# Kernel tuning notes

Measured on AMD Instinct MI355X. Metric: run time of the kernel, lower is better.

Reference implementation:

```python
import jax, jax.numpy as jnp
import numpy as np


def _ramp_filter(sino):
    # Ram-Lak ramp filter along detector columns (last axis), applied in Fourier
    # space. Equivalent to projector.filter_projections, vectorized over batch.
    n = sino.shape[-1]
    ramp = (2.0 * jnp.abs(jnp.fft.fftfreq(n))).astype(sino.dtype)  # [C]
    f = jnp.fft.fft(sino, axis=-1)
    return jnp.real(jnp.fft.ifft(f * ramp, axis=-1)).astype(sino.dtype)


def _fbp(sino):
    # sino: [B, V, R, C] -> image [B, R, C, C]
    B, V, R, C = sino.shape
    filt = _ramp_filter(sino)
    npix = C
    half = (npix - 1) / 2.0
    coords = jnp.arange(npix, dtype=sino.dtype) - half
    X = coords[None, :]          # image x, broadcasts to [npix, npix]
    Y = coords[:, None]          # image y
    angles = jnp.linspace(0.0, np.pi, V, endpoint=False).astype(sino.dtype)
    dcenter = (C - 1) / 2.0

    def body(acc, inputs):
        proj, theta = inputs                      # proj: [B, R, C]
        t = X * jnp.cos(theta) + Y * jnp.sin(theta) + dcenter  # [npix, npix]
        t = jnp.clip(t, 0.0, C - 1)
        i0 = jnp.floor(t).astype(jnp.int32)
        i1 = jnp.minimum(i0 + 1, C - 1)
        w = (t - i0).astype(proj.dtype)
        g0 = proj[:, :, i0]                       # gather -> [B, R, npix, npix]
        g1 = proj[:, :, i1]
        return acc + g0 * (1.0 - w) + g1 * w, None

    init = jnp.zeros((B, R, npix, npix), sino.dtype)
    projT = jnp.moveaxis(filt, 1, 0)              # [V, B, R, C]
    acc, _ = jax.lax.scan(body, init, (projT, angles))
    img = acc * (np.pi / V)
    return jnp.maximum(img, 0.0)                  # img[img < 0] = 0


def setup_inputs() -> dict:
    key = jax.random.key(0)
    B, V, R, C = 2, 180, 32, 512
    sino = jax.random.normal(key, (B, V, R, C), dtype=jnp.float32)
    return {"sino": sino}


def reference(sino):
    return _fbp(sino)
```

## Files before the change

### kernel.cpp

```cpp
#include <hip/hip_runtime.h>
#include <math.h>

#ifndef M_PI
#define M_PI 3.14159265358979323846
#endif

#define BB 2
#define VV 180
#define RR 32
#define CC 512
#define NPIX 512

#define PADL 106
#define PW 724
#define TCEN 362

#define SH3 8
#define CHP 2
#define NCHP 45

#define SH 16
#define CH2 6
#define NCHUNK2 30

#define TAB_OFF 2048
#define FILT_OFF 2048

__global__ void precompute_kernel(float* __restrict__ ws) {
    int j = blockIdx.x * blockDim.x + threadIdx.x;
    if (j < 512) {
        float s = 0.f;
        for (int m = 1; m < 512; ++m) {
            int p = (m * j) & 511;
            float ang = (float)(2.0 * M_PI / 512.0) * (float)p;
            int mm = m < 512 - m ? m : 512 - m;
            float ramp = 2.0f * (float)mm * (1.0f / 512.0f);
            s += ramp * cosf(ang);
        }
        s *= (1.0f / 512.0f);
        s *= (float)(M_PI / (double)VV);
        ws[j] = s;
        ws[j + 512] = s;
    }
    if (j < VV) {
        float th = (float)((double)j * M_PI / 180.0);
        float c = cosf(th), sn = sinf(th);
        ws[1024 + j] = c;
        ws[1024 + 180 + j] = sn;
        ws[1408 + 2 * j] = c;
        ws[1408 + 2 * j + 1] = sn;
    }
}

__global__ __launch_bounds__(128) void conv_table_kernel(const float* __restrict__ sino,
                                                         const float* __restrict__ ws,
                                                         float* __restrict__ table) {
    __shared__ float rows_s[16 * 512];
    __shared__ float h_s[1024];
    int t = threadIdx.x;
    int blk = blockIdx.x;
    int bv = blk >> 1;
    int half = blk & 1;
    int b = bv / 180;
    int v = bv - b * 180;

    const float4* src4 = (const float4*)(sino + (((size_t)bv * 32) + (size_t)half * 16) * 512);
    float4* rows4 = (float4*)rows_s;
    for (int i = t; i < 2048; i += 128) rows4[i] = src4[i];
    for (int i = t; i < 1024; i += 128) h_s[i] = ws[i];
    __syncthreads();

    int wave = t >> 6;
    int lane = t & 63;
    int row0 = wave * 8;

    float acc[8][8];
#pragma unroll
    for (int j = 0; j < 8; ++j)
#pragma unroll
        for (int i = 0; i < 8; ++i) acc[j][i] = 0.f;

    for (int k = 0; k < 512; k += 4) {
        float4 rv[8];
#pragma unroll
        for (int j = 0; j < 8; ++j)
            rv[j] = *(const float4*)&rows_s[(row0 + j) * 512 + k];
#pragma unroll
        for (int u = 0; u < 4; ++u) {
            float hv[8];
            int base = lane - (k + u) + 512;
#pragma unroll
            for (int i = 0; i < 8; ++i) hv[i] = h_s[base + 64 * i];
#pragma unroll
            for (int j = 0; j < 8; ++j) {
                float rj = (u == 0) ? rv[j].x : (u == 1) ? rv[j].y : (u == 2) ? rv[j].z : rv[j].w;
#pragma unroll
                for (int i = 0; i < 8; ++i) acc[j][i] = fmaf(rj, hv[i], acc[j][i]);
            }
        }
    }

    __syncthreads();
#pragma unroll
    for (int j = 0; j < 8; ++j)
#pragma unroll
        for (int i = 0; i < 8; ++i)
            rows_s[(row0 + j) * 512 + lane + 64 * i] = acc[j][i];
    __syncthreads();

    int p = (v < 90) ? v : v - 90;
    size_t halfByte = (v < 90) ? 0 : 8;
    for (int jj = 0; jj < 16; ++jj) {
        const float* fr = rows_s + jj * 512;
        int slice = b * 32 + half * 16 + jj;
        char* trow = (char*)table + (((size_t)slice * 90 + p) * PW) * 16 + halfByte;
        for (int cx = t; cx < PW; cx += 128) {
            int s0 = cx - PADL;
            int i0 = min(max(s0, 0), 511);
            int i1 = min(max(s0 + 1, 0), 511);
            float f0 = fr[i0];
            float d = fr[i1] - f0;
            float m = (float)(cx - TCEN);
            *(float2*)(trow + (size_t)cx * 16) = make_float2(fmaf(-m, d, f0), d);
        }
    }
}

__global__ __launch_bounds__(256, 6) void backproj_pair_kernel(const float4* __restrict__ tab,
                                                               const float2* __restrict__ trigp,
                                                               float* __restrict__ out) {
    __shared__ float4 pbuf[CHP * PW];
    __shared__ float2 trig_s[90];
    int t = threadIdx.x;
    int slice = blockIdx.y;
    int strip = blockIdx.x;
    int y0 = strip * SH3;
    const float4* tslice = tab + (size_t)slice * (90 * PW);

    for (int i = t; i < 90; i += 256) trig_s[i] = trigp[i];

    float xc = (float)t + 0.5f;

    float acc0[SH3], acc1[SH3], acc2[SH3], acc3[SH3];
#pragma unroll
    for (int j = 0; j < SH3; ++j) { acc0[j] = 0.f; acc1[j] = 0.f; acc2[j] = 0.f; acc3[j] = 0.f; }

    for (int chunk = 0; chunk < NCHP; ++chunk) {
        __syncthreads();
        const float4* src = tslice + chunk * (CHP * PW);
        for (int i = t; i < CHP * PW; i += 256) pbuf[i] = src[i];
        __syncthreads();
#pragma unroll
        for (int pa = 0; pa < CHP; ++pa) {
            float2 cs = trig_s[chunk * CHP + pa];
            const float4* pb = pbuf + pa * PW + TCEN;
#pragma unroll
            for (int j = 0; j < SH3; ++j) {
                float ycj = (float)(y0 + j) + 0.5f;
                float ysm  = fmaf(ycj, cs.y, -0.5f);
                float yccm = fmaf(-ycj, cs.x, -0.5f);
                float ua  = fmaf(xc, cs.x, ysm);
                float ub  = fmaf(xc, cs.y, yccm);
                float uma = -1.0f - ua;
                float umb = -1.0f - ub;
                int ma  = (int)floorf(ua);
                int mma = (int)floorf(uma);
                int mb  = (int)floorf(ub);
                int mmb = (int)floorf(umb);
                float4 qa  = pb[ma];
                float4 qma = pb[mma];
                float4 qb  = pb[mb];
                float4 qmb = pb[mmb];
                acc0[j] = fmaf(ua,  qa.y,  acc0[j]) + qa.x;
                acc1[j] = fmaf(ua,  qa.w,  acc1[j]) + qa.z;
                acc2[j] = fmaf(uma, qma.y, acc2[j]) + qma.x;
                acc3[j] = fmaf(uma, qma.w, acc3[j]) + qma.z;
                acc1[j] = fmaf(ub,  qb.y,  acc1[j]) + qb.x;
                acc2[j] = fmaf(ub,  qb.w,  acc2[j]) + qb.z;
                acc3[j] = fmaf(umb, qmb.y, acc3[j]) + qmb.x;
                acc0[j] = fmaf(umb, qmb.w, acc0[j]) + qmb.z;
            }
        }
    }

    int px = 256 + t;
    size_t sbase = (size_t)slice * (512 * 512);
#pragma unroll
    for (int j = 0; j < SH3; ++j) {
        int py = 256 + y0 + j;
        float v0 = acc0[j], v1 = acc1[j], v2 = acc2[j], v3 = acc3[j];
        out[sbase + (size_t)py * 512 + px]                   = v0 > 0.f ? v0 : 0.f;
        out[sbase + (size_t)px * 512 + (511 - py)]           = v1 > 0.f ? v1 : 0.f;
        out[sbase + (size_t)(511 - py) * 512 + (511 - px)]   = v2 > 0.f ? v2 : 0.f;
        out[sbase + (size_t)(511 - px) * 512 + py]           = v3 > 0.f ? v3 : 0.f;
    }
}

__global__ __launch_bounds__(128) void conv_kernel(const float* __restrict__ sino,
                                                   const float* __restrict__ ws,
                                                   float* __restrict__ filt) {
    __shared__ float rows_s[16 * 512];
    __shared__ float h_s[1024];
    int t = threadIdx.x;
    int blk = blockIdx.x;
    int bv = blk >> 1;
    int half = blk & 1;
    int b = bv / 180;
    int v = bv - b * 180;

    const float4* src4 = (const float4*)(sino + (((size_t)bv * 32) + (size_t)half * 16) * 512);
    float4* rows4 = (float4*)rows_s;
    for (int i = t; i < 2048; i += 128) rows4[i] = src4[i];
    for (int i = t; i < 1024; i += 128) h_s[i] = ws[i];
    __syncthreads();

    int wave = t >> 6;
    int lane = t & 63;
    int row0 = wave * 8;

    float acc[8][8];
#pragma unroll
    for (int j = 0; j < 8; ++j)
#pragma unroll
        for (int i = 0; i < 8; ++i) acc[j][i] = 0.f;

    for (int k = 0; k < 512; k += 4) {
        float4 rv[8];
#pragma unroll
        for (int j = 0; j < 8; ++j)
            rv[j] = *(const float4*)&rows_s[(row0 + j) * 512 + k];
#pragma unroll
        for (int u = 0; u < 4; ++u) {
            float hv[8];
            int base = lane - (k + u) + 512;
#pragma unroll
            for (int i = 0; i < 8; ++i) hv[i] = h_s[base + 64 * i];
#pragma unroll
            for (int j = 0; j < 8; ++j) {
                float rj = (u == 0) ? rv[j].x : (u == 1) ? rv[j].y : (u == 2) ? rv[j].z : rv[j].w;
#pragma unroll
                for (int i = 0; i < 8; ++i) acc[j][i] = fmaf(rj, hv[i], acc[j][i]);
            }
        }
    }

#pragma unroll
    for (int j = 0; j < 8; ++j) {
        int r = half * 16 + row0 + j;
        float* dst = filt + (((size_t)b * 32 + r) * 180 + v) * 512;
#pragma unroll
        for (int i = 0; i < 8; ++i) dst[lane + 64 * i] = acc[j][i];
    }
}

__global__ __launch_bounds__(256) void backproj_kernel(const float* __restrict__ filt,
                                                       const float* __restrict__ trig,
                                                       float* __restrict__ out) {
    __shared__ float2 pbuf[CH2][PW];
    __shared__ float trig_s[360];
    int t = threadIdx.x;
    int slice = blockIdx.y;
    int strip = blockIdx.x;
    int y0 = strip * SH;
    int lane = t & 63;
    int wave = t >> 6;
    int x0 = wave * 128;
    const float* slice_p = filt + (size_t)slice * (180 * 512);

    for (int i = t; i < 360; i += 256) trig_s[i] = trig[i];

    float xc0 = (float)(x0 + lane) - 255.5f;
    float xc1 = xc0 + 64.0f;
    float yb0 = (float)y0 - 255.5f;

    float acc[2][SH];
#pragma unroll
    for (int g = 0; g < 2; ++g)
#pragma unroll
        for (int j = 0; j < SH; ++j) acc[g][j] = 0.f;

    for (int chunk = 0; chunk < NCHUNK2; ++chunk) {
        int v0 = chunk * CH2;
        __syncthreads();
#pragma unroll 1
        for (int a = 0; a < CH2; ++a) {
            const float* prow = slice_p + (v0 + a) * 512;
            for (int cx = t; cx < PW; cx += 256) {
                int s0 = cx - PADL;
                int i0 = min(max(s0, 0), 511);
                int i1 = min(max(s0 + 1, 0), 511);
                float f0 = prow[i0];
                float d = prow[i1] - f0;
                float m = (float)(cx - TCEN);
                pbuf[a][cx] = make_float2(fmaf(-m, d, f0), d);
            }
        }
        __syncthreads();
#pragma unroll 1
        for (int a = 0; a < CH2; ++a) {
            float cth = trig_s[v0 + a];
            float sth = trig_s[180 + v0 + a];
            float ybase = fmaf(yb0, sth, 255.5f + (float)PADL - (float)TCEN);
            float t0 = fmaf(xc0, cth, ybase);
            float t1 = fmaf(xc1, cth, ybase);
            const char* pb = (const char*)pbuf;
            int aoff = a * (PW * 8) + TCEN * 8;
#pragma unroll
            for (int j = 0; j < SH; ++j) {
                int m0 = (int)floorf(t0);
                float2 g0 = *(const float2*)(pb + (m0 * 8 + aoff));
                acc[0][j] = fmaf(t0, g0.y, acc[0][j]) + g0.x;
                t0 += sth;

                int m1 = (int)floorf(t1);
                float2 g1 = *(const float2*)(pb + (m1 * 8 + aoff));
                acc[1][j] = fmaf(t1, g1.y, acc[1][j]) + g1.x;
                t1 += sth;
            }
        }
    }

    size_t obase = ((size_t)slice * 512 + (size_t)y0) * 512;
#pragma unroll
    for (int j = 0; j < SH; ++j) {
        float v0o = acc[0][j];
        float v1o = acc[1][j];
        out[obase + (size_t)j * 512 + x0 + lane] = v0o > 0.f ? v0o : 0.f;
        out[obase + (size_t)j * 512 + x0 + 64 + lane] = v1o > 0.f ? v1o : 0.f;
    }
}

extern "C" void kernel_launch(void* const* d_in, const int* in_sizes, int n_in,
                              void* d_out, int out_size, void* d_ws, size_t ws_size,
                              hipStream_t stream) {
    const float* sino = (const float*)d_in[0];
    float* out = (float*)d_out;
    float* ws = (float*)d_ws;

    size_t tableFloats = (size_t)64 * 90 * PW * 4;
    size_t needed = (TAB_OFF + tableFloats) * sizeof(float);

    precompute_kernel<<<2, 256, 0, stream>>>(ws);
    if (ws_size >= needed) {
        float* table = ws + TAB_OFF;
        conv_table_kernel<<<720, 128, 0, stream>>>(sino, ws, table);
        backproj_pair_kernel<<<dim3(32, 64), 256, 0, stream>>>((const float4*)table,
                                                               (const float2*)(ws + 1408), out);
    } else {
        float* filt = ws + FILT_OFF;
        conv_kernel<<<720, 128, 0, stream>>>(sino, ws, filt);
        backproj_kernel<<<dim3(32, 64), 256, 0, stream>>>(filt, ws + 1024, out);
    }
}
```

Baseline: 682.7 us.

## Store backprojection table in fp16 and vectorize convolution filter loads

The per-angle interpolation table drops from four fp32 values to packed half-precision base and delta pairs, halving the table that backprojection streams into shared memory and its global footprint. Backprojection now computes the fractional weight explicitly and unpacks halves to float. The convolution also reads a precomputed float4 of four shifted filter taps per load, cutting shared-memory reads per FMA, at the cost of a small extra kernel. The fp16 storage lowers the precision of the filtered projections.

```diff
diff --git a/kernel.cpp b/kernel.cpp
--- a/kernel.cpp
+++ b/kernel.cpp
@@ -1,4 +1,5 @@
 #include <hip/hip_runtime.h>
+#include <hip/hip_fp16.h>
 #include <math.h>
 
 #ifndef M_PI
@@ -23,7 +24,8 @@
 #define CH2 6
 #define NCHUNK2 30
 
-#define TAB_OFF 2048
+#define H4_OFF 2048
+#define TAB_OFF 6144
 #define FILT_OFF 2048
 
 __global__ void precompute_kernel(float* __restrict__ ws) {
@@ -52,11 +54,23 @@
     }
 }
 
+__global__ void precompute_h4_kernel(float* __restrict__ ws) {
+    int x = blockIdx.x * blockDim.x + threadIdx.x;
+    if (x < 1024) {
+        float4 h4;
+        h4.x = ws[x];
+        h4.y = ws[(x - 1) & 1023];
+        h4.z = ws[(x - 2) & 1023];
+        h4.w = ws[(x - 3) & 1023];
+        *(float4*)(ws + H4_OFF + 4 * x) = h4;
+    }
+}
+
 __global__ __launch_bounds__(128) void conv_table_kernel(const float* __restrict__ sino,
                                                          const float* __restrict__ ws,
-                                                         float* __restrict__ table) {
+                                                         unsigned int* __restrict__ table) {
     __shared__ float rows_s[16 * 512];
-    __shared__ float h_s[1024];
+    __shared__ float4 h4_s[1024];
     int t = threadIdx.x;
     int blk = blockIdx.x;
     int bv = blk >> 1;
@@ -67,7 +81,8 @@
     const float4* src4 = (const float4*)(sino + (((size_t)bv * 32) + (size_t)half * 16) * 512);
     float4* rows4 = (float4*)rows_s;
     for (int i = t; i < 2048; i += 128) rows4[i] = src4[i];
-    for (int i = t; i < 1024; i += 128) h_s[i] = ws[i];
+    const float4* h4g = (const float4*)(ws + H4_OFF);
+    for (int i = t; i < 1024; i += 128) h4_s[i] = h4g[i];
     __syncthreads();
 
     int wave = t >> 6;
@@ -85,17 +100,20 @@
 #pragma unroll
         for (int j = 0; j < 8; ++j)
             rv[j] = *(const float4*)&rows_s[(row0 + j) * 512 + k];
-#pragma unroll
-        for (int u = 0; u < 4; ++u) {
-            float hv[8];
-            int base = lane - (k + u) + 512;
-#pragma unroll
-            for (int i = 0; i < 8; ++i) hv[i] = h_s[base + 64 * i];
-#pragma unroll
-            for (int j = 0; j < 8; ++j) {
-                float rj = (u == 0) ? rv[j].x : (u == 1) ? rv[j].y : (u == 2) ? rv[j].z : rv[j].w;
-#pragma unroll
-                for (int i = 0; i < 8; ++i) acc[j][i] = fmaf(rj, hv[i], acc[j][i]);
+        float4 hq[8];
+#pragma unroll
+        for (int i = 0; i < 8; ++i)
+            hq[i] = h4_s[lane - k + 512 + 64 * i];
+#pragma unroll
+        for (int j = 0; j < 8; ++j) {
+#pragma unroll
+            for (int i = 0; i < 8; ++i) {
+                float a = acc[j][i];
+                a = fmaf(rv[j].x, hq[i].x, a);
+                a = fmaf(rv[j].y, hq[i].y, a);
+                a = fmaf(rv[j].z, hq[i].z, a);
+                a = fmaf(rv[j].w, hq[i].w, a);
+                acc[j][i] = a;
             }
         }
     }
@@ -109,33 +127,42 @@
     __syncthreads();
 
     int p = (v < 90) ? v : v - 90;
-    size_t halfByte = (v < 90) ? 0 : 8;
+    int word = (v < 90) ? 0 : 1;
     for (int jj = 0; jj < 16; ++jj) {
         const float* fr = rows_s + jj * 512;
         int slice = b * 32 + half * 16 + jj;
-        char* trow = (char*)table + (((size_t)slice * 90 + p) * PW) * 16 + halfByte;
+        unsigned int* trow = table + (((size_t)slice * 90 + p) * PW) * 2 + word;
         for (int cx = t; cx < PW; cx += 128) {
             int s0 = cx - PADL;
             int i0 = min(max(s0, 0), 511);
             int i1 = min(max(s0 + 1, 0), 511);
             float f0 = fr[i0];
-            float d = fr[i1] - f0;
-            float m = (float)(cx - TCEN);
-            *(float2*)(trow + (size_t)cx * 16) = make_float2(fmaf(-m, d, f0), d);
-        }
-    }
-}
-
-__global__ __launch_bounds__(256, 6) void backproj_pair_kernel(const float4* __restrict__ tab,
+            float f1 = fr[i1];
+            __half h0 = __float2half_rn(f0);
+            __half h1 = __float2half_rn(f1);
+            __half hd = __float2half_rn(__half2float(h1) - __half2float(h0));
+            unsigned int packed = ((unsigned int)__half_as_ushort(hd) << 16) |
+                                  (unsigned int)__half_as_ushort(h0);
+            trow[(size_t)cx * 2] = packed;
+        }
+    }
+}
+
+static __device__ inline float2 unpack_h2(unsigned int u) {
+    __half2 h = *reinterpret_cast<__half2*>(&u);
+    return __half22float2(h);
+}
+
+__global__ __launch_bounds__(256, 6) void backproj_pair_kernel(const uint2* __restrict__ tab,
                                                                const float2* __restrict__ trigp,
                                                                float* __restrict__ out) {
-    __shared__ float4 pbuf[CHP * PW];
+    __shared__ uint2 pbuf[CHP * PW];
     __shared__ float2 trig_s[90];
     int t = threadIdx.x;
     int slice = blockIdx.y;
     int strip = blockIdx.x;
     int y0 = strip * SH3;
-    const float4* tslice = tab + (size_t)slice * (90 * PW);
+    const uint2* tslice = tab + (size_t)slice * (90 * PW);
 
     for (int i = t; i < 90; i += 256) trig_s[i] = trigp[i];
 
@@ -147,13 +174,14 @@
 
     for (int chunk = 0; chunk < NCHP; ++chunk) {
         __syncthreads();
-        const float4* src = tslice + chunk * (CHP * PW);
-        for (int i = t; i < CHP * PW; i += 256) pbuf[i] = src[i];
+        const float4* src = (const float4*)(tslice + chunk * (CHP * PW));
+        float4* dst = (float4*)pbuf;
+        for (int i = t; i < (CHP * PW) / 2; i += 256) dst[i] = src[i];
         __syncthreads();
 #pragma unroll
         for (int pa = 0; pa < CHP; ++pa) {
             float2 cs = trig_s[chunk * CHP + pa];
-            const float4* pb = pbuf + pa * PW + TCEN;
+            const uint2* pb = pbuf + pa * PW + TCEN;
 #pragma unroll
             for (int j = 0; j < SH3; ++j) {
                 float ycj = (float)(y0 + j) + 0.5f;
@@ -161,24 +189,36 @@
                 float yccm = fmaf(-ycj, cs.x, -0.5f);
                 float ua  = fmaf(xc, cs.x, ysm);
                 float ub  = fmaf(xc, cs.y, yccm);
-                float uma = -1.0f - ua;
-                float umb = -1.0f - ub;
-                int ma  = (int)floorf(ua);
-                int mma = (int)floorf(uma);
-                int mb  = (int)floorf(ub);
-                int mmb = (int)floorf(umb);
-                float4 qa  = pb[ma];
-                float4 qma = pb[mma];
-                float4 qb  = pb[mb];
-                float4 qmb = pb[mmb];
-                acc0[j] = fmaf(ua,  qa.y,  acc0[j]) + qa.x;
-                acc1[j] = fmaf(ua,  qa.w,  acc1[j]) + qa.z;
-                acc2[j] = fmaf(uma, qma.y, acc2[j]) + qma.x;
-                acc3[j] = fmaf(uma, qma.w, acc3[j]) + qma.z;
-                acc1[j] = fmaf(ub,  qb.y,  acc1[j]) + qb.x;
-                acc2[j] = fmaf(ub,  qb.w,  acc2[j]) + qb.z;
-                acc3[j] = fmaf(umb, qmb.y, acc3[j]) + qmb.x;
-                acc0[j] = fmaf(umb, qmb.w, acc0[j]) + qmb.z;
+                float fla = floorf(ua);
+                float flb = floorf(ub);
+                int ma  = (int)fla;
+                int mb  = (int)flb;
+                float ra = ua - fla;
+                float rb = ub - flb;
+                int mma = -2 - ma;
+                int mmb = -2 - mb;
+                float rma = 1.0f - ra;
+                float rmb = 1.0f - rb;
+                uint2 qa  = pb[ma];
+                uint2 qma = pb[mma];
+                uint2 qb  = pb[mb];
+                uint2 qmb = pb[mmb];
+                float2 av  = unpack_h2(qa.x);
+                float2 aw  = unpack_h2(qa.y);
+                acc0[j] += fmaf(ra,  av.y, av.x);
+                acc1[j] += fmaf(ra,  aw.y, aw.x);
+                float2 mav = unpack_h2(qma.x);
+                float2 maw = unpack_h2(qma.y);
+                acc2[j] += fmaf(rma, mav.y, mav.x);
+                acc3[j] += fmaf(rma, maw.y, maw.x);
+                float2 bv  = unpack_h2(qb.x);
+                float2 bw  = unpack_h2(qb.y);
+                acc1[j] += fmaf(rb,  bv.y, bv.x);
+                acc2[j] += fmaf(rb,  bw.y, bw.x);
+                float2 mbv = unpack_h2(qmb.x);
+                float2 mbw = unpack_h2(qmb.y);
+                acc3[j] += fmaf(rmb, mbv.y, mbv.x);
+                acc0[j] += fmaf(rmb, mbw.y, mbw.x);
             }
         }
     }
@@ -337,14 +377,15 @@
     float* out = (float*)d_out;
     float* ws = (float*)d_ws;
 
-    size_t tableFloats = (size_t)64 * 90 * PW * 4;
-    size_t needed = (TAB_OFF + tableFloats) * sizeof(float);
+    size_t tableWords = (size_t)64 * 90 * PW * 2;
+    size_t needed = ((size_t)TAB_OFF + tableWords) * 4;
 
     precompute_kernel<<<2, 256, 0, stream>>>(ws);
     if (ws_size >= needed) {
-        float* table = ws + TAB_OFF;
+        unsigned int* table = (unsigned int*)(ws + TAB_OFF);
+        precompute_h4_kernel<<<4, 256, 0, stream>>>(ws);
         conv_table_kernel<<<720, 128, 0, stream>>>(sino, ws, table);
-        backproj_pair_kernel<<<dim3(32, 64), 256, 0, stream>>>((const float4*)table,
+        backproj_pair_kernel<<<dim3(32, 64), 256, 0, stream>>>((const uint2*)table,
                                                                (const float2*)(ws + 1408), out);
     } else {
         float* filt = ws + FILT_OFF;
```

Result: no change. 682.1 us (-0.1%).
